# Optimization experiments

Measured on AMD Instinct MI355X. Metric: run time of the kernel, lower is better.

Reference implementation:

```python
import math
import jax, jax.numpy as jnp
import numpy as np

B, L, D = 2, 2048, 2048
H, DH = 16, 128
DFF = 8192


def setup_inputs() -> dict:
    key = jax.random.key(0)
    ks = jax.random.split(key, 9)
    x = jax.random.normal(ks[0], (B, L, D), dtype=jnp.float32)
    # additive causal mask: 0 on/below diagonal, -inf above
    neg = jnp.finfo(jnp.float32).min
    mask = jnp.where(jnp.tril(jnp.ones((L, L), dtype=bool)), 0.0, neg)[None, None]
    s = 0.02
    return {
        "x": x,
        "mask": mask,
        "ln1_w": jnp.ones((D,), jnp.float32),
        "wq": jax.random.normal(ks[1], (D, D), jnp.float32) * s,
        "wk": jax.random.normal(ks[2], (D, D), jnp.float32) * s,
        "wv": jax.random.normal(ks[3], (D, D), jnp.float32) * s,
        "wo": jax.random.normal(ks[4], (D, D), jnp.float32) * s,
        "ln2_w": jnp.ones((D,), jnp.float32),
        "w_up": jax.random.normal(ks[5], (DFF, D), jnp.float32) * s,
        "w_down": jax.random.normal(ks[6], (D, DFF), jnp.float32) * s,
    }


def _rmsnorm(x, w, eps=1e-8):
    rms = jnp.sqrt(jnp.mean(x * x, axis=-1, keepdims=True) + eps)
    return x / rms * w


def reference(x, mask, ln1_w, wq, wk, wv, wo, ln2_w, w_up, w_down):
    h = _rmsnorm(x, ln1_w)
    # torch Linear: y = x @ W.T ; weights are [out, in]
    q = (h @ wq.T).reshape(B, L, H, DH).transpose(0, 2, 1, 3)  # [B,H,L,DH]
    k = (h @ wk.T).reshape(B, L, H, DH).transpose(0, 2, 1, 3)
    v = (h @ wv.T).reshape(B, L, H, DH).transpose(0, 2, 1, 3)
    scores = jnp.einsum('bhqd,bhkd->bhqk', q, k) / math.sqrt(DH)
    scores = scores + mask
    attn = jax.nn.softmax(scores, axis=-1)
    out = jnp.einsum('bhqk,bhkd->bhqd', attn, v)
    out = out.transpose(0, 2, 1, 3).reshape(B, L, D)
    x = x + out @ wo.T
    h = _rmsnorm(x, ln2_w)
    ff = jax.nn.gelu(h @ w_up.T, approximate=False) @ w_down.T  # exact erf GELU as in F.gelu
    return x + ff
```

## Files before the change

### kernel.cpp

```cpp
#include <hip/hip_runtime.h>
#include <hip/hip_bf16.h>
#include <math.h>

#define B_   2
#define L_   2048
#define D_   2048
#define H_   16
#define DH_  128
#define DFF_ 8192
#define NTOK (B_*L_)

typedef __attribute__((ext_vector_type(8))) short bf16x8;
typedef __attribute__((ext_vector_type(4))) float floatx4;
typedef unsigned short u16;

__device__ __forceinline__ u16 f2bf(float f) {
    union { float f; unsigned u; } c; c.f = f;
    unsigned r = (c.u + 0x7fffu + ((c.u >> 16) & 1u)) >> 16;
    return (u16)r;
}

__device__ __forceinline__ void async_cp16(const u16* g, u16* l) {
    __builtin_amdgcn_global_load_lds(
        (const __attribute__((address_space(1))) unsigned int*)g,
        (__attribute__((address_space(3))) unsigned int*)l,
        16, 0, 0);
}

__global__ __launch_bounds__(256) void cvt_bf16(const float* __restrict__ in,
                                                u16* __restrict__ out, int n4) {
    int i = blockIdx.x * 256 + threadIdx.x;
    if (i >= n4) return;
    float4 v = ((const float4*)in)[i];
    ushort4 o = { f2bf(v.x), f2bf(v.y), f2bf(v.z), f2bf(v.w) };
    ((ushort4*)out)[i] = o;
}

__global__ __launch_bounds__(256) void rmsnorm_kernel(const float* __restrict__ x,
                                                      const float* __restrict__ w,
                                                      u16* __restrict__ out) {
    const int row = blockIdx.x, tid = threadIdx.x;
    const float* xr = x + (size_t)row * D_;
    float4 a = ((const float4*)xr)[tid];
    float4 b = ((const float4*)xr)[tid + 256];
    float ss = a.x*a.x + a.y*a.y + a.z*a.z + a.w*a.w
             + b.x*b.x + b.y*b.y + b.z*b.z + b.w*b.w;
#pragma unroll
    for (int d = 1; d < 64; d <<= 1) ss += __shfl_xor(ss, d, 64);
    __shared__ float sred[4];
    if ((tid & 63) == 0) sred[tid >> 6] = ss;
    __syncthreads();
    float tot = sred[0] + sred[1] + sred[2] + sred[3];
    float inv = 1.0f / sqrtf(tot * (1.0f / D_) + 1e-8f);
    float4 w0 = ((const float4*)w)[tid];
    float4 w1 = ((const float4*)w)[tid + 256];
    ushort4 o0 = { f2bf(a.x*inv*w0.x), f2bf(a.y*inv*w0.y), f2bf(a.z*inv*w0.z), f2bf(a.w*inv*w0.w) };
    ushort4 o1 = { f2bf(b.x*inv*w1.x), f2bf(b.y*inv*w1.y), f2bf(b.z*inv*w1.z), f2bf(b.w*inv*w1.w) };
    ushort4* orow = (ushort4*)(out + (size_t)row * D_);
    orow[tid] = o0;
    orow[tid + 256] = o1;
}

template<int MODE>
__global__ __launch_bounds__(256) void gemm_bt(const u16* __restrict__ A,
                                               const u16* __restrict__ Bw,
                                               void* __restrict__ outp,
                                               const float* __restrict__ residual,
                                               int M, int N, int K, float scale) {
    __shared__ __attribute__((aligned(16))) u16 lds_a[128 * 32];
    __shared__ __attribute__((aligned(16))) u16 lds_b[128 * 32];
    const int tid = threadIdx.x;
    const int wave = tid >> 6, lane = tid & 63;
    const int qd = lane >> 4, c16 = lane & 15;
    const int wm = (wave >> 1) * 64, wn = (wave & 1) * 64;
    const long tile_m = (long)blockIdx.y * 128, tile_n = (long)blockIdx.x * 128;

    floatx4 acc[4][4] = {};

    const int r0 = tid >> 2;
    const int r1 = r0 + 64;
    const int kc = (tid & 3) * 8;
    const u16* a0 = A + (tile_m + r0) * (long)K + kc;
    const u16* a1 = A + (tile_m + r1) * (long)K + kc;
    const u16* b0 = Bw + (tile_n + r0) * (long)K + kc;
    const u16* b1 = Bw + (tile_n + r1) * (long)K + kc;

    for (int k0 = 0; k0 < K; k0 += 32) {
        async_cp16(a0 + k0, &lds_a[r0 * 32 + kc]);
        async_cp16(a1 + k0, &lds_a[r1 * 32 + kc]);
        async_cp16(b0 + k0, &lds_b[r0 * 32 + kc]);
        async_cp16(b1 + k0, &lds_b[r1 * 32 + kc]);
        __syncthreads();
        bf16x8 af[4], bv[4];
#pragma unroll
        for (int i = 0; i < 4; i++)
            af[i] = *(const bf16x8*)&lds_a[(wm + i * 16 + c16) * 32 + qd * 8];
#pragma unroll
        for (int j = 0; j < 4; j++)
            bv[j] = *(const bf16x8*)&lds_b[(wn + j * 16 + c16) * 32 + qd * 8];
#pragma unroll
        for (int i = 0; i < 4; i++)
#pragma unroll
            for (int j = 0; j < 4; j++)
                acc[i][j] = __builtin_amdgcn_mfma_f32_16x16x32_bf16(af[i], bv[j], acc[i][j], 0, 0, 0);
        __syncthreads();
    }

#pragma unroll
    for (int i = 0; i < 4; i++) {
#pragma unroll
        for (int j = 0; j < 4; j++) {
#pragma unroll
            for (int r = 0; r < 4; r++) {
                long m = tile_m + wm + i * 16 + qd * 4 + r;
                long n = tile_n + wn + j * 16 + c16;
                float v = acc[i][j][r];
                if (MODE == 0) {
                    long b = m >> 11, l = m & 2047;
                    long h = n >> 7, dh = n & 127;
                    ((u16*)outp)[((b * H_ + h) * (long)L_ + l) * DH_ + dh] = f2bf(v * scale);
                } else if (MODE == 1) {
                    long idx = m * (long)N + n;
                    ((float*)outp)[idx] = v + residual[idx];
                } else if (MODE == 2) {
                    float g = 0.5f * v * (1.0f + erff(v * 0.70710678118654752f));
                    ((u16*)outp)[m * (long)N + n] = f2bf(g);
                } else {
                    ((u16*)outp)[m * (long)N + n] = f2bf(v);
                }
            }
        }
    }
}

#define KSTRIDE 136
#define VSTRIDE 72
#define PSTRIDE 72
__global__ __launch_bounds__(256) void attn_kernel(const u16* __restrict__ Q,
                                                   const u16* __restrict__ K,
                                                   const u16* __restrict__ VT,
                                                   u16* __restrict__ O) {
    __shared__ __attribute__((aligned(16))) u16 kt_lds[64 * KSTRIDE];
    __shared__ __attribute__((aligned(16))) u16 vt_lds[128 * VSTRIDE];
    __shared__ __attribute__((aligned(16))) u16 p_lds[4][16 * PSTRIDE];
    const int tid = threadIdx.x;
    const int wave = tid >> 6, lane = tid & 63;
    const int qd = lane >> 4, c16 = lane & 15;
    const int pair = blockIdx.x, bh = blockIdx.y;
    const int b = bh >> 4, h = bh & 15;
    const u16* qh = Q + (size_t)bh * L_ * DH_;
    const u16* kh = K + (size_t)bh * L_ * DH_;
    const u16* vth = VT + (size_t)h * DH_ * NTOK + (size_t)b * L_;

    for (int qsel = 0; qsel < 2; ++qsel) {
        const int qt = qsel ? (31 - pair) : pair;
        const int q0 = qt * 64;

        bf16x8 qf[4];
#pragma unroll
        for (int s = 0; s < 4; s++)
            qf[s] = *(const bf16x8*)(qh + (size_t)(q0 + wave * 16 + c16) * DH_ + s * 32 + qd * 8);

        floatx4 o_acc[8] = {};
        float m_i[4], l_i[4];
#pragma unroll
        for (int r = 0; r < 4; r++) { m_i[r] = -1e30f; l_i[r] = 0.f; }

        for (int kt = 0; kt <= qt; kt++) {
            const int kv0 = kt * 64;
#pragma unroll
            for (int s = 0; s < 4; s++) {
                int c = tid + s * 256;
                int kr = c >> 4, koff = (c & 15) * 8;
                *(int4*)&kt_lds[kr * KSTRIDE + koff] =
                    *(const int4*)(kh + (size_t)(kv0 + kr) * DH_ + koff);
                int dh = c >> 3, kv8 = (c & 7) * 8;
                *(int4*)&vt_lds[dh * VSTRIDE + kv8] =
                    *(const int4*)(vth + (size_t)dh * NTOK + kv0 + kv8);
            }
            __syncthreads();

            floatx4 s_acc[4] = {};
#pragma unroll
            for (int j = 0; j < 4; j++)
#pragma unroll
                for (int s = 0; s < 4; s++) {
                    bf16x8 kf = *(const bf16x8*)&kt_lds[(j * 16 + c16) * KSTRIDE + s * 32 + qd * 8];
                    s_acc[j] = __builtin_amdgcn_mfma_f32_16x16x32_bf16(qf[s], kf, s_acc[j], 0, 0, 0);
                }

            if (kt == qt) {
#pragma unroll
                for (int j = 0; j < 4; j++)
#pragma unroll
                    for (int r = 0; r < 4; r++) {
                        int col = j * 16 + c16;
                        int row = wave * 16 + qd * 4 + r;
                        if (col > row) s_acc[j][r] = -1e30f;
                    }
            }

            float rsum[4], alpha[4];
#pragma unroll
            for (int r = 0; r < 4; r++) {
                float mx = fmaxf(fmaxf(s_acc[0][r], s_acc[1][r]), fmaxf(s_acc[2][r], s_acc[3][r]));
#pragma unroll
                for (int d = 1; d < 16; d <<= 1) mx = fmaxf(mx, __shfl_xor(mx, d, 64));
                float mnew = fmaxf(m_i[r], mx);
                alpha[r] = __expf(m_i[r] - mnew);
                m_i[r] = mnew;
                rsum[r] = 0.f;
            }
#pragma unroll
            for (int j = 0; j < 4; j++)
#pragma unroll
                for (int r = 0; r < 4; r++) {
                    float p = __expf(s_acc[j][r] - m_i[r]);
                    s_acc[j][r] = p;
                    rsum[r] += p;
                }
#pragma unroll
            for (int r = 0; r < 4; r++) {
#pragma unroll
                for (int d = 1; d < 16; d <<= 1) rsum[r] += __shfl_xor(rsum[r], d, 64);
                l_i[r] = l_i[r] * alpha[r] + rsum[r];
            }
#pragma unroll
            for (int j8 = 0; j8 < 8; j8++)
#pragma unroll
                for (int r = 0; r < 4; r++) o_acc[j8][r] *= alpha[r];

#pragma unroll
            for (int j = 0; j < 4; j++)
#pragma unroll
                for (int r = 0; r < 4; r++)
                    p_lds[wave][(qd * 4 + r) * PSTRIDE + j * 16 + c16] = f2bf(s_acc[j][r]);

#pragma unroll
            for (int s = 0; s < 2; s++) {
                bf16x8 pf = *(const bf16x8*)&p_lds[wave][c16 * PSTRIDE + s * 32 + qd * 8];
#pragma unroll
                for (int j8 = 0; j8 < 8; j8++) {
                    bf16x8 vf = *(const bf16x8*)&vt_lds[(j8 * 16 + c16) * VSTRIDE + s * 32 + qd * 8];
                    o_acc[j8] = __builtin_amdgcn_mfma_f32_16x16x32_bf16(pf, vf, o_acc[j8], 0, 0, 0);
                }
            }
            __syncthreads();
        }

        float inv_l[4];
#pragma unroll
        for (int r = 0; r < 4; r++) inv_l[r] = 1.0f / l_i[r];
#pragma unroll
        for (int j8 = 0; j8 < 8; j8++)
#pragma unroll
            for (int r = 0; r < 4; r++) {
                int l = q0 + wave * 16 + qd * 4 + r;
                int d = h * DH_ + j8 * 16 + c16;
                O[(size_t)(b * L_ + l) * D_ + d] = f2bf(o_acc[j8][r] * inv_l[r]);
            }
    }
}

extern "C" void kernel_launch(void* const* d_in, const int* in_sizes, int n_in,
                              void* d_out, int out_size, void* d_ws, size_t ws_size,
                              hipStream_t stream) {
    const float* x     = (const float*)d_in[0];
    const float* ln1_w = (const float*)d_in[2];
    const float* wq    = (const float*)d_in[3];
    const float* wk    = (const float*)d_in[4];
    const float* wv    = (const float*)d_in[5];
    const float* wo    = (const float*)d_in[6];
    const float* ln2_w = (const float*)d_in[7];
    const float* w_up  = (const float*)d_in[8];
    const float* w_dn  = (const float*)d_in[9];

    char* ws = (char*)d_ws;
    const size_t MB = 1024 * 1024;
    float* x2   = (float*)(ws + 0);
    u16* hbuf   = (u16*)(ws + 32 * MB);
    u16* qbuf   = (u16*)(ws + 48 * MB);
    u16* kbuf   = (u16*)(ws + 64 * MB);
    u16* vtbuf  = (u16*)(ws + 80 * MB);
    u16* attnb  = (u16*)(ws + 96 * MB);
    u16* upbuf  = (u16*)(ws + 48 * MB);
    u16* wbufA  = (u16*)(ws + 112 * MB);
    u16* wbufB  = (u16*)(ws + 120 * MB);
    u16* wbufC  = (u16*)(ws + 128 * MB);

    dim3 blk(256);
    const int nW = D_ * D_;
    const int nU = DFF_ * D_;
    cvt_bf16<<<(nW / 4 + 255) / 256, blk, 0, stream>>>(wq, wbufA, nW / 4);
    cvt_bf16<<<(nW / 4 + 255) / 256, blk, 0, stream>>>(wk, wbufB, nW / 4);
    cvt_bf16<<<(nW / 4 + 255) / 256, blk, 0, stream>>>(wv, wbufC, nW / 4);
    rmsnorm_kernel<<<NTOK, blk, 0, stream>>>(x, ln1_w, hbuf);

    dim3 g1(D_ / 128, NTOK / 128);
    gemm_bt<0><<<g1, blk, 0, stream>>>(hbuf, wbufA, qbuf, nullptr, NTOK, D_, D_, 0.08838834764831845f);
    gemm_bt<0><<<g1, blk, 0, stream>>>(hbuf, wbufB, kbuf, nullptr, NTOK, D_, D_, 1.0f);
    dim3 gv(NTOK / 128, D_ / 128);
    gemm_bt<3><<<gv, blk, 0, stream>>>(wbufC, hbuf, vtbuf, nullptr, D_, NTOK, D_, 1.0f);

    dim3 ga(16, B_ * H_);
    attn_kernel<<<ga, blk, 0, stream>>>(qbuf, kbuf, vtbuf, attnb);

    cvt_bf16<<<(nW / 4 + 255) / 256, blk, 0, stream>>>(wo, wbufA, nW / 4);
    gemm_bt<1><<<g1, blk, 0, stream>>>(attnb, wbufA, x2, x, NTOK, D_, D_, 1.0f);

    rmsnorm_kernel<<<NTOK, blk, 0, stream>>>(x2, ln2_w, hbuf);

    cvt_bf16<<<(nU / 4 + 255) / 256, blk, 0, stream>>>(w_up, wbufA, nU / 4);
    dim3 g2(DFF_ / 128, NTOK / 128);
    gemm_bt<2><<<g2, blk, 0, stream>>>(hbuf, wbufA, upbuf, nullptr, NTOK, DFF_, D_, 1.0f);

    cvt_bf16<<<(nU / 4 + 255) / 256, blk, 0, stream>>>(w_dn, wbufA, nU / 4);
    gemm_bt<1><<<g1, blk, 0, stream>>>(upbuf, wbufA, (float*)d_out, x2, NTOK, D_, DFF_, 1.0f);
}
```

Measured before the change: 955.5 us.

## Fuse Q/K projections into one GEMM and deepen GEMM k-step to 64

The Q and K weight matrices are converted into adjacent buffers and computed by a single GEMM launch with N=2*D. The epilogue routes each column to the Q or K buffer and applies the softmax scale only to Q. The GEMM main loop now loads two 32-wide K slices per barrier pair into separate LDS buffers, which halves the number of synchronizations. The cost is twice the LDS per block, which may lower occupancy, and all loads are still issued before the barrier, so there is no real overlap.

```diff
diff --git a/kernel.cpp b/kernel.cpp
--- a/kernel.cpp
+++ b/kernel.cpp
@@ -65,10 +65,11 @@
 __global__ __launch_bounds__(256) void gemm_bt(const u16* __restrict__ A,
                                                const u16* __restrict__ Bw,
                                                void* __restrict__ outp,
+                                               void* __restrict__ outp2,
                                                const float* __restrict__ residual,
                                                int M, int N, int K, float scale) {
-    __shared__ __attribute__((aligned(16))) u16 lds_a[128 * 32];
-    __shared__ __attribute__((aligned(16))) u16 lds_b[128 * 32];
+    __shared__ __attribute__((aligned(16))) u16 lds_a[2][128 * 32];
+    __shared__ __attribute__((aligned(16))) u16 lds_b[2][128 * 32];
     const int tid = threadIdx.x;
     const int wave = tid >> 6, lane = tid & 63;
     const int qd = lane >> 4, c16 = lane & 15;
@@ -85,24 +86,31 @@
     const u16* b0 = Bw + (tile_n + r0) * (long)K + kc;
     const u16* b1 = Bw + (tile_n + r1) * (long)K + kc;
 
-    for (int k0 = 0; k0 < K; k0 += 32) {
-        async_cp16(a0 + k0, &lds_a[r0 * 32 + kc]);
-        async_cp16(a1 + k0, &lds_a[r1 * 32 + kc]);
-        async_cp16(b0 + k0, &lds_b[r0 * 32 + kc]);
-        async_cp16(b1 + k0, &lds_b[r1 * 32 + kc]);
+    for (int k0 = 0; k0 < K; k0 += 64) {
+#pragma unroll
+        for (int p = 0; p < 2; p++) {
+            const int kp = k0 + p * 32;
+            async_cp16(a0 + kp, &lds_a[p][r0 * 32 + kc]);
+            async_cp16(a1 + kp, &lds_a[p][r1 * 32 + kc]);
+            async_cp16(b0 + kp, &lds_b[p][r0 * 32 + kc]);
+            async_cp16(b1 + kp, &lds_b[p][r1 * 32 + kc]);
+        }
         __syncthreads();
-        bf16x8 af[4], bv[4];
-#pragma unroll
-        for (int i = 0; i < 4; i++)
-            af[i] = *(const bf16x8*)&lds_a[(wm + i * 16 + c16) * 32 + qd * 8];
-#pragma unroll
-        for (int j = 0; j < 4; j++)
-            bv[j] = *(const bf16x8*)&lds_b[(wn + j * 16 + c16) * 32 + qd * 8];
-#pragma unroll
-        for (int i = 0; i < 4; i++)
+#pragma unroll
+        for (int p = 0; p < 2; p++) {
+            bf16x8 af[4], bv[4];
+#pragma unroll
+            for (int i = 0; i < 4; i++)
+                af[i] = *(const bf16x8*)&lds_a[p][(wm + i * 16 + c16) * 32 + qd * 8];
 #pragma unroll
             for (int j = 0; j < 4; j++)
-                acc[i][j] = __builtin_amdgcn_mfma_f32_16x16x32_bf16(af[i], bv[j], acc[i][j], 0, 0, 0);
+                bv[j] = *(const bf16x8*)&lds_b[p][(wn + j * 16 + c16) * 32 + qd * 8];
+#pragma unroll
+            for (int i = 0; i < 4; i++)
+#pragma unroll
+                for (int j = 0; j < 4; j++)
+                    acc[i][j] = __builtin_amdgcn_mfma_f32_16x16x32_bf16(af[i], bv[j], acc[i][j], 0, 0, 0);
+        }
         __syncthreads();
     }
 
@@ -117,8 +125,11 @@
                 float v = acc[i][j][r];
                 if (MODE == 0) {
                     long b = m >> 11, l = m & 2047;
-                    long h = n >> 7, dh = n & 127;
-                    ((u16*)outp)[((b * H_ + h) * (long)L_ + l) * DH_ + dh] = f2bf(v * scale);
+                    int isq = n < D_;
+                    long f = n & 2047, h = f >> 7, dh = f & 127;
+                    u16* dst = isq ? (u16*)outp : (u16*)outp2;
+                    dst[((b * H_ + h) * (long)L_ + l) * DH_ + dh] =
+                        f2bf(v * (isq ? scale : 1.0f));
                 } else if (MODE == 1) {
                     long idx = m * (long)N + n;
                     ((float*)outp)[idx] = v + residual[idx];
@@ -285,35 +296,35 @@
     u16* attnb  = (u16*)(ws + 96 * MB);
     u16* upbuf  = (u16*)(ws + 48 * MB);
     u16* wbufA  = (u16*)(ws + 112 * MB);
-    u16* wbufB  = (u16*)(ws + 120 * MB);
     u16* wbufC  = (u16*)(ws + 128 * MB);
 
     dim3 blk(256);
     const int nW = D_ * D_;
     const int nU = DFF_ * D_;
     cvt_bf16<<<(nW / 4 + 255) / 256, blk, 0, stream>>>(wq, wbufA, nW / 4);
-    cvt_bf16<<<(nW / 4 + 255) / 256, blk, 0, stream>>>(wk, wbufB, nW / 4);
+    cvt_bf16<<<(nW / 4 + 255) / 256, blk, 0, stream>>>(wk, wbufA + (size_t)nW, nW / 4);
     cvt_bf16<<<(nW / 4 + 255) / 256, blk, 0, stream>>>(wv, wbufC, nW / 4);
     rmsnorm_kernel<<<NTOK, blk, 0, stream>>>(x, ln1_w, hbuf);
 
-    dim3 g1(D_ / 128, NTOK / 128);
-    gemm_bt<0><<<g1, blk, 0, stream>>>(hbuf, wbufA, qbuf, nullptr, NTOK, D_, D_, 0.08838834764831845f);
-    gemm_bt<0><<<g1, blk, 0, stream>>>(hbuf, wbufB, kbuf, nullptr, NTOK, D_, D_, 1.0f);
+    dim3 gqk(2 * D_ / 128, NTOK / 128);
+    gemm_bt<0><<<gqk, blk, 0, stream>>>(hbuf, wbufA, qbuf, kbuf, nullptr,
+                                        NTOK, 2 * D_, D_, 0.08838834764831845f);
     dim3 gv(NTOK / 128, D_ / 128);
-    gemm_bt<3><<<gv, blk, 0, stream>>>(wbufC, hbuf, vtbuf, nullptr, D_, NTOK, D_, 1.0f);
+    gemm_bt<3><<<gv, blk, 0, stream>>>(wbufC, hbuf, vtbuf, nullptr, nullptr, D_, NTOK, D_, 1.0f);
 
     dim3 ga(16, B_ * H_);
     attn_kernel<<<ga, blk, 0, stream>>>(qbuf, kbuf, vtbuf, attnb);
 
     cvt_bf16<<<(nW / 4 + 255) / 256, blk, 0, stream>>>(wo, wbufA, nW / 4);
-    gemm_bt<1><<<g1, blk, 0, stream>>>(attnb, wbufA, x2, x, NTOK, D_, D_, 1.0f);
+    dim3 g1(D_ / 128, NTOK / 128);
+    gemm_bt<1><<<g1, blk, 0, stream>>>(attnb, wbufA, x2, nullptr, x, NTOK, D_, D_, 1.0f);
 
     rmsnorm_kernel<<<NTOK, blk, 0, stream>>>(x2, ln2_w, hbuf);
 
     cvt_bf16<<<(nU / 4 + 255) / 256, blk, 0, stream>>>(w_up, wbufA, nU / 4);
     dim3 g2(DFF_ / 128, NTOK / 128);
-    gemm_bt<2><<<g2, blk, 0, stream>>>(hbuf, wbufA, upbuf, nullptr, NTOK, DFF_, D_, 1.0f);
+    gemm_bt<2><<<g2, blk, 0, stream>>>(hbuf, wbufA, upbuf, nullptr, nullptr, NTOK, DFF_, D_, 1.0f);
 
     cvt_bf16<<<(nU / 4 + 255) / 256, blk, 0, stream>>>(w_dn, wbufA, nU / 4);
-    gemm_bt<1><<<g1, blk, 0, stream>>>(upbuf, wbufA, (float*)d_out, x2, NTOK, D_, DFF_, 1.0f);
-}
+    gemm_bt<1><<<g1, blk, 0, stream>>>(upbuf, wbufA, (float*)d_out, nullptr, x2, NTOK, D_, DFF_, 1.0f);
+}
```

Measured after the change: 873.5 us. -8.6%, faster.
